# Performance work log

Hardware: AMD Instinct MI355X
Metric: run time of the kernel (lower is better)

## Reference

```python
import jax, jax.numpy as jnp
import numpy as np

DEPTH, DIM, HEADS, DHEAD, MLP, CTX_DIM = 4, 1024, 16, 64, 4096, 1024
INNER = HEADS * DHEAD
SCALE = DHEAD ** -0.5
B, N, M = 4, 1024, 2048


def setup_inputs() -> dict:
    key = jax.random.key(0)
    ks = jax.random.split(key, 16)
    w = lambda k, shape: jax.random.normal(k, shape, dtype=jnp.float32) * 0.02
    return {
        "x": jax.random.normal(ks[0], (B, N, DIM), dtype=jnp.float32),
        "context": jax.random.normal(ks[1], (B, M, CTX_DIM), dtype=jnp.float32),
        "mask": jnp.ones((B, N), dtype=jnp.int32),
        # LayerNorm params: index 0 = pre-self-attn, 1 = pre-cross-attn, 2 = pre-FFN
        "ln_g": jnp.ones((DEPTH, 3, DIM), dtype=jnp.float32),
        "ln_b": jnp.zeros((DEPTH, 3, DIM), dtype=jnp.float32),
        "Wqkv": w(ks[2], (DEPTH, DIM, 3 * INNER)),
        "Wo_sa": w(ks[3], (DEPTH, INNER, DIM)),
        "bo_sa": jnp.zeros((DEPTH, DIM), dtype=jnp.float32),
        "Wkv": w(ks[4], (DEPTH, CTX_DIM, 2 * INNER)),
        "Wq": w(ks[5], (DEPTH, DIM, INNER)),
        "Wo_ca": w(ks[6], (DEPTH, INNER, DIM)),
        "bo_ca": jnp.zeros((DEPTH, DIM), dtype=jnp.float32),
        "W1": w(ks[7], (DEPTH, DIM, MLP)),
        "b1": jnp.zeros((DEPTH, MLP), dtype=jnp.float32),
        "W2": w(ks[8], (DEPTH, MLP, DIM)),
        "b2": jnp.zeros((DEPTH, DIM), dtype=jnp.float32),
    }


def _ln(x, g, b, eps=1e-5):
    mu = jnp.mean(x, axis=-1, keepdims=True)
    var = jnp.var(x, axis=-1, keepdims=True)
    return (x - mu) * jax.lax.rsqrt(var + eps) * g + b


def _split_heads(t):  # [b, n, h*d] -> [b, h, n, d]
    b, n, _ = t.shape
    return t.reshape(b, n, HEADS, DHEAD).transpose(0, 2, 1, 3)


def _merge_heads(t):  # [b, h, n, d] -> [b, n, h*d]
    b, h, n, d = t.shape
    return t.transpose(0, 2, 1, 3).reshape(b, n, h * d)


def _forward(x, context, mask, ln_g, ln_b, Wqkv, Wo_sa, bo_sa, Wkv, Wq, Wo_ca, bo_ca, W1, b1, W2, b2):
    neg_mask = (1 - mask).astype(x.dtype)  # [b, n]
    for i in range(DEPTH):
        # ---- self-attention (PreNorm) ----
        h = _ln(x, ln_g[i, 0], ln_b[i, 0])
        qkv = h @ Wqkv[i]
        q, k, v = jnp.split(qkv, 3, axis=-1)
        q, k, v = _split_heads(q), _split_heads(k), _split_heads(v)
        dots = jnp.einsum('bhnd,bhmd->bhnm', q, k) * SCALE
        dots = dots - neg_mask[:, None, None, :] * 1e11  # mask over keys
        attn = jax.nn.softmax(dots, axis=-1)
        out = _merge_heads(jnp.einsum('bhnm,bhmd->bhnd', attn, v))
        x = x + out @ Wo_sa[i] + bo_sa[i]
        # ---- cross-attention (PreNorm) ----
        h = _ln(x, ln_g[i, 1], ln_b[i, 1])
        kv = context @ Wkv[i]
        k, v = jnp.split(kv, 2, axis=-1)
        q = _split_heads(h @ Wq[i])
        k, v = _split_heads(k), _split_heads(v)
        dots = jnp.einsum('bhnd,bhmd->bhnm', q, k) * SCALE  # [b, h, n, m]
        dots = dots - neg_mask[:, None, :, None] * 1e6  # mask over queries
        attn = jax.nn.softmax(dots, axis=-1)
        out = _merge_heads(jnp.einsum('bhnm,bhmd->bhnd', attn, v))
        x = x + out @ Wo_ca[i] + bo_ca[i]
        # ---- feed-forward (PreNorm) ----
        h = _ln(x, ln_g[i, 2], ln_b[i, 2])
        h = jax.nn.gelu(h @ W1[i] + b1[i], approximate=False)
        x = x + h @ W2[i] + b2[i]
    return x


def reference(x, context, mask, ln_g, ln_b, Wqkv, Wo_sa, bo_sa, Wkv, Wq, Wo_ca, bo_ca, W1, b1, W2, b2):
    return _forward(x, context, mask, ln_g, ln_b, Wqkv, Wo_sa, bo_sa, Wkv, Wq, Wo_ca, bo_ca, W1, b1, W2, b2)
```

## Files before the change

### kernel.cpp

```cpp
#include <hip/hip_runtime.h>
#include <math.h>

#define DEPTH_ 4
#define DIM_ 1024
#define HEADS_ 16
#define DHEAD_ 64
#define MLP_ 4096
#define CTX_ 1024
#define INNER_ 1024
#define B_ 4
#define N_ 1024
#define M_ 2048

typedef unsigned short u16;
typedef __attribute__((ext_vector_type(4))) unsigned short u16x4;
typedef __attribute__((ext_vector_type(8))) short bf16x8;
typedef __attribute__((ext_vector_type(4))) float f32x4;
typedef __attribute__((ext_vector_type(4))) int i32x4;

#define SCQ 0.18033688011112042f

__device__ __forceinline__ u16 f2bf(float f) {
    unsigned u = __float_as_uint(f);
    return (u16)((u + 0x7fffu + ((u >> 16) & 1u)) >> 16);
}

__device__ __forceinline__ float bf2f(u16 v) {
    return __uint_as_float(((unsigned)v) << 16);
}

__device__ __forceinline__ float exp2_fast(float x) {
    float r;
    asm("v_exp_f32 %0, %1" : "=v"(r) : "v"(x));
    return r;
}

__device__ __forceinline__ float rcp_fast(float x) {
    float r;
    asm("v_rcp_f32 %0, %1" : "=v"(r) : "v"(x));
    return r;
}

__device__ __forceinline__ float max3f(float a, float b, float c) {
    float r;
    asm("v_max3_f32 %0, %1, %2, %3" : "=v"(r) : "v"(a), "v"(b), "v"(c));
    return r;
}

__device__ __forceinline__ unsigned cvt_pk_bf16(float lo, float hi) {
    unsigned r;
    asm("v_cvt_pk_bf16_f32 %0, %1, %2" : "=v"(r) : "v"(lo), "v"(hi));
    return r;
}

__device__ __forceinline__ float gelu_fast(float v) {
    float t = v + 0.044715f * v * v * v;
    float e = exp2_fast(-2.302221673f * t);
    return v * rcp_fast(1.0f + e);
}

__device__ __forceinline__ int kv_sigma(int kv) {
    return (kv & ~31) | (((kv >> 2) & 3) << 3) | (((kv >> 4) & 1) << 2) |
           (kv & 3);
}

#define GLOAD16(gp, sp)                                                        \
    __builtin_amdgcn_global_load_lds(                                          \
        (const __attribute__((address_space(1))) void*)(gp),                   \
        (__attribute__((address_space(3))) void*)(sp), 16, 0, 0)

template <int MODE>
__global__ __launch_bounds__(256) void ln_res(
    u16* __restrict__ xb, const u16* __restrict__ d0,
    const u16* __restrict__ d1, const float* __restrict__ dbias,
    const float* __restrict__ g, const float* __restrict__ b,
    u16* __restrict__ y) {
    int row = blockIdx.x;
    u16x4 xv = ((const u16x4*)(xb + (size_t)row * DIM_))[threadIdx.x];
    float4 v = {bf2f(xv[0]), bf2f(xv[1]), bf2f(xv[2]), bf2f(xv[3])};
    if constexpr (MODE == 1) {
        u16x4 a0 = ((const u16x4*)(d0 + (size_t)row * DIM_))[threadIdx.x];
        u16x4 a1 = ((const u16x4*)(d1 + (size_t)row * DIM_))[threadIdx.x];
        float4 bb4 = ((const float4*)dbias)[threadIdx.x];
        v.x += bf2f(a0[0]) + bf2f(a1[0]) + bb4.x;
        v.y += bf2f(a0[1]) + bf2f(a1[1]) + bb4.y;
        v.z += bf2f(a0[2]) + bf2f(a1[2]) + bb4.z;
        v.w += bf2f(a0[3]) + bf2f(a1[3]) + bb4.w;
        u16x4 xo = {f2bf(v.x), f2bf(v.y), f2bf(v.z), f2bf(v.w)};
        ((u16x4*)(xb + (size_t)row * DIM_))[threadIdx.x] = xo;
    }
    float s  = v.x + v.y + v.z + v.w;
    float ss = v.x * v.x + v.y * v.y + v.z * v.z + v.w * v.w;
    #pragma unroll
    for (int off = 32; off; off >>= 1) {
        s  += __shfl_down(s, off);
        ss += __shfl_down(ss, off);
    }
    __shared__ float red[10];
    int wid = threadIdx.x >> 6, lane = threadIdx.x & 63;
    if (lane == 0) { red[wid] = s; red[4 + wid] = ss; }
    __syncthreads();
    if (threadIdx.x == 0) {
        float ts  = red[0] + red[1] + red[2] + red[3];
        float tss = red[4] + red[5] + red[6] + red[7];
        float mu  = ts * (1.0f / DIM_);
        float var = tss * (1.0f / DIM_) - mu * mu;
        red[8] = mu;
        red[9] = rsqrtf(var + 1e-5f);
    }
    __syncthreads();
    float mu = red[8], rs = red[9];
    float4 gg = ((const float4*)g)[threadIdx.x];
    float4 bb = ((const float4*)b)[threadIdx.x];
    u16x4 o;
    o[0] = f2bf((v.x - mu) * rs * gg.x + bb.x);
    o[1] = f2bf((v.y - mu) * rs * gg.y + bb.y);
    o[2] = f2bf((v.z - mu) * rs * gg.z + bb.z);
    o[3] = f2bf((v.w - mu) * rs * gg.w + bb.w);
    ((u16x4*)(y + (size_t)row * DIM_))[threadIdx.x] = o;
}

__global__ __launch_bounds__(256) void res_add(
    float* __restrict__ xout, const u16* __restrict__ xb,
    const u16* __restrict__ d0, const u16* __restrict__ d1,
    const float* __restrict__ dbias) {
    int row = blockIdx.x;
    u16x4 xv = ((const u16x4*)(xb + (size_t)row * DIM_))[threadIdx.x];
    u16x4 a0 = ((const u16x4*)(d0 + (size_t)row * DIM_))[threadIdx.x];
    u16x4 a1 = ((const u16x4*)(d1 + (size_t)row * DIM_))[threadIdx.x];
    float4 bb4 = ((const float4*)dbias)[threadIdx.x];
    float4 v;
    v.x = bf2f(xv[0]) + bf2f(a0[0]) + bf2f(a1[0]) + bb4.x;
    v.y = bf2f(xv[1]) + bf2f(a0[1]) + bf2f(a1[1]) + bb4.y;
    v.z = bf2f(xv[2]) + bf2f(a0[2]) + bf2f(a1[2]) + bb4.z;
    v.w = bf2f(xv[3]) + bf2f(a0[3]) + bf2f(a1[3]) + bb4.w;
    ((float4*)(xout + (size_t)row * DIM_))[threadIdx.x] = v;
}

__global__ __launch_bounds__(256) void cast_kernel(const float* __restrict__ in,
                                                   u16* __restrict__ out) {
    int i = blockIdx.x * 256 + threadIdx.x;
    float4 v = ((const float4*)in)[i];
    u16x4 o = {f2bf(v.x), f2bf(v.y), f2bf(v.z), f2bf(v.w)};
    ((u16x4*)out)[i] = o;
}

struct PrepArgs {
    const float* src[7];
    int K[7];
    int N[7];
    int dstOff[7];
    int tileCum[7];
};

__global__ __launch_bounds__(256) void prep_weights(PrepArgs a,
                                                    u16* __restrict__ wt) {
    __shared__ float tile[32][33];
    int bid = blockIdx.x;
    int wi = 0;
    while (bid >= a.tileCum[wi]) ++wi;
    int tbase = wi ? a.tileCum[wi - 1] : 0;
    int tid = bid - tbase;
    int Kd = a.K[wi], Nd = a.N[wi];
    int ntx = Nd >> 5;
    int bx = (tid % ntx) * 32;
    int by = (tid / ntx) * 32;
    const float* W = a.src[wi];
    u16* Wt = wt + a.dstOff[wi];

    int t = threadIdx.x;
    int kl = t >> 3, n4 = (t & 7) * 4;
    float4 v = *(const float4*)(W + (size_t)(by + kl) * Nd + bx + n4);
    tile[kl][n4 + 0] = v.x; tile[kl][n4 + 1] = v.y;
    tile[kl][n4 + 2] = v.z; tile[kl][n4 + 3] = v.w;
    __syncthreads();
    int nl = t >> 3, k4 = (t & 7) * 4;
    u16x4 o;
    #pragma unroll
    for (int j = 0; j < 4; ++j) o[j] = f2bf(tile[k4 + j][nl]);
    *(u16x4*)(Wt + (size_t)(bx + nl) * Kd + by + k4) = o;
}

template <int EPI, int SPLITK>
__global__ __launch_bounds__(256, 3) void gemm_mfma3(
    const u16* __restrict__ A, const u16* __restrict__ Bt,
    const float* __restrict__ bias, void* __restrict__ Cout,
    u16* __restrict__ vt, int Mdim, int Ndim, int Kdim, int nx, int ny) {
    __shared__ __align__(16) u16 As[3][128 * 32];
    __shared__ __align__(16) u16 Bs[3][128 * 32];
    const int t = threadIdx.x;
    const int lane = t & 63, w = t >> 6;
    const int c = lane & 15, g = lane >> 4;
    const int wy = w >> 1, wx = w & 1;

    const int nwg = gridDim.x;
    const int wid = (blockIdx.x & 7) * (nwg >> 3) + (blockIdx.x >> 3);
    const int bx = wid % nx;
    const int by = (wid / nx) % ny;
    const int bz = wid / (nx * ny);
    const int m0 = by * 128, n0 = bx * 128;

    f32x4 acc[4][4] = {};

    const int srow = w * 32 + (lane >> 2);
    const int scb  = (((lane & 3) ^ ((srow >> 1) & 3)) * 8);
    const u16* Ag = A + (size_t)(m0 + srow) * Kdim + scb;
    const u16* Bg = Bt + (size_t)(n0 + srow) * Kdim + scb;

    auto stage = [&](int buf, int k0) {
        GLOAD16(Ag + k0, &As[buf][w * 1024]);
        GLOAD16(Ag + k0 + (size_t)16 * Kdim, &As[buf][w * 1024 + 512]);
        GLOAD16(Bg + k0, &Bs[buf][w * 1024]);
        GLOAD16(Bg + k0 + (size_t)16 * Kdim, &Bs[buf][w * 1024 + 512]);
    };
    const int rsw = (c >> 1) & 3;
    auto compute = [&](int buf) {
        bf16x8 a[4], b[4];
        #pragma unroll
        for (int i = 0; i < 4; ++i)
            a[i] = *(const bf16x8*)&As[buf][(wy * 64 + i * 16 + c) * 32 +
                                            ((g ^ rsw) * 8)];
        #pragma unroll
        for (int j = 0; j < 4; ++j)
            b[j] = *(const bf16x8*)&Bs[buf][(wx * 64 + j * 16 + c) * 32 +
                                            ((g ^ rsw) * 8)];
        __builtin_amdgcn_s_setprio(1);
        #pragma unroll
        for (int i = 0; i < 4; ++i)
            #pragma unroll
            for (int j = 0; j < 4; ++j)
                acc[i][j] = __builtin_amdgcn_mfma_f32_16x16x32_bf16(
                    a[i], b[j], acc[i][j], 0, 0, 0);
        __builtin_amdgcn_s_setprio(0);
    };

    const int kchunk = Kdim / SPLITK;
    const int kbeg = bz * kchunk;
    const int nsteps = kchunk / 32;

    stage(0, kbeg);
    stage(1, kbeg + 32);
    int cb = 0, sb = 2;
    for (int s = 0; s < nsteps; ++s) {
        if (s + 1 < nsteps)
            asm volatile("s_waitcnt vmcnt(4)" ::: "memory");
        else
            asm volatile("s_waitcnt vmcnt(0)" ::: "memory");
        __builtin_amdgcn_s_barrier();
        if (s + 2 < nsteps) {
            stage(sb, kbeg + (s + 2) * 32);
            sb = (sb == 2) ? 0 : sb + 1;
        }
        compute(cb);
        cb = (cb == 2) ? 0 : cb + 1;
    }

    const size_t outOff = (SPLITK > 1) ? (size_t)bz * Mdim * Ndim : 0;

    #pragma unroll
    for (int i = 0; i < 4; ++i) {
        int row0 = m0 + wy * 64 + i * 16 + g * 4;
        #pragma unroll
        for (int j = 0; j < 4; ++j) {
            int col = n0 + wx * 64 + j * 16 + c;
            u16x4 o4;
            #pragma unroll
            for (int r = 0; r < 4; ++r) {
                float v = acc[i][j][r];
                size_t idx = (size_t)(row0 + r) * Ndim + col;
                if constexpr (EPI == 0) {
                    ((u16*)Cout)[outOff + idx] = f2bf(v);
                } else if constexpr (EPI == 4) {
                    if (col < 1024) v *= SCQ;
                    u16 bv = f2bf(v);
                    ((u16*)Cout)[idx] = bv;
                    o4[r] = bv;
                } else if constexpr (EPI == 1) {
                    v += bias[col];
                    ((u16*)Cout)[idx] = f2bf(gelu_fast(v));
                }
            }
            if constexpr (EPI == 4) {
                if (n0 + wx * 64 + j * 16 >= 2048) {
                    int hh = (col - 2048) >> 6;
                    int dd = col & 63;
                    int bi = row0 / 1024;
                    int kv = row0 % 1024;
                    int kvs = kv_sigma(kv);
                    *(u16x4*)&vt[(((size_t)bi * HEADS_ + hh) * 64 + dd) * 1024 +
                                 kvs] = o4;
                }
            }
        }
    }
}

__global__ __launch_bounds__(256, 3) void gemm_dual(
    const u16* __restrict__ Akv, const u16* __restrict__ Btkv,
    u16* __restrict__ Ckv, u16* __restrict__ vt,
    const u16* __restrict__ Aq, const u16* __restrict__ Btq,
    u16* __restrict__ Cq) {
    __shared__ __align__(16) u16 As[3][128 * 32];
    __shared__ __align__(16) u16 Bs[3][128 * 32];
    const int t = threadIdx.x;
    const int lane = t & 63, w = t >> 6;
    const int c = lane & 15, g = lane >> 4;
    const int wy = w >> 1, wx = w & 1;
    const int Kdim = 1024;

    const int nwg = gridDim.x;
    const int wid = (blockIdx.x & 7) * (nwg >> 3) + (blockIdx.x >> 3);
    const bool pkv = wid < 1024;
    const u16* A;
    const u16* Bt;
    u16* Cc;
    int Ndim, bx, by;
    if (pkv) {
        A = Akv; Bt = Btkv; Cc = Ckv; Ndim = 2048;
        bx = wid & 15; by = wid >> 4;
    } else {
        int w2 = wid - 1024;
        A = Aq; Bt = Btq; Cc = Cq; Ndim = 1024;
        bx = w2 & 7; by = w2 >> 3;
    }
    const int m0 = by * 128, n0 = bx * 128;

    f32x4 acc[4][4] = {};

    const int srow = w * 32 + (lane >> 2);
    const int scb  = (((lane & 3) ^ ((srow >> 1) & 3)) * 8);
    const u16* Ag = A + (size_t)(m0 + srow) * Kdim + scb;
    const u16* Bg = Bt + (size_t)(n0 + srow) * Kdim + scb;

    auto stage = [&](int buf, int k0) {
        GLOAD16(Ag + k0, &As[buf][w * 1024]);
        GLOAD16(Ag + k0 + (size_t)16 * Kdim, &As[buf][w * 1024 + 512]);
        GLOAD16(Bg + k0, &Bs[buf][w * 1024]);
        GLOAD16(Bg + k0 + (size_t)16 * Kdim, &Bs[buf][w * 1024 + 512]);
    };
    const int rsw = (c >> 1) & 3;
    auto compute = [&](int buf) {
        bf16x8 a[4], b[4];
        #pragma unroll
        for (int i = 0; i < 4; ++i)
            a[i] = *(const bf16x8*)&As[buf][(wy * 64 + i * 16 + c) * 32 +
                                            ((g ^ rsw) * 8)];
        #pragma unroll
        for (int j = 0; j < 4; ++j)
            b[j] = *(const bf16x8*)&Bs[buf][(wx * 64 + j * 16 + c) * 32 +
                                            ((g ^ rsw) * 8)];
        __builtin_amdgcn_s_setprio(1);
        #pragma unroll
        for (int i = 0; i < 4; ++i)
            #pragma unroll
            for (int j = 0; j < 4; ++j)
                acc[i][j] = __builtin_amdgcn_mfma_f32_16x16x32_bf16(
                    a[i], b[j], acc[i][j], 0, 0, 0);
        __builtin_amdgcn_s_setprio(0);
    };

    stage(0, 0);
    stage(1, 32);
    int cb = 0, sb = 2;
    const int nsteps = 32;
    for (int s = 0; s < nsteps; ++s) {
        if (s + 1 < nsteps)
            asm volatile("s_waitcnt vmcnt(4)" ::: "memory");
        else
            asm volatile("s_waitcnt vmcnt(0)" ::: "memory");
        __builtin_amdgcn_s_barrier();
        if (s + 2 < nsteps) {
            stage(sb, (s + 2) * 32);
            sb = (sb == 2) ? 0 : sb + 1;
        }
        compute(cb);
        cb = (cb == 2) ? 0 : cb + 1;
    }

    #pragma unroll
    for (int i = 0; i < 4; ++i) {
        int row0 = m0 + wy * 64 + i * 16 + g * 4;
        #pragma unroll
        for (int j = 0; j < 4; ++j) {
            int col = n0 + wx * 64 + j * 16 + c;
            u16x4 o4;
            #pragma unroll
            for (int r = 0; r < 4; ++r) {
                float v = acc[i][j][r];
                size_t idx = (size_t)(row0 + r) * Ndim + col;
                if (pkv) {
                    u16 bv = f2bf(v);
                    Cc[idx] = bv;
                    o4[r] = bv;
                } else {
                    Cc[idx] = f2bf(v * SCQ);
                }
            }
            if (pkv && (n0 + wx * 64 + j * 16 >= 1024)) {
                int hh = (col - 1024) >> 6;
                int dd = col & 63;
                int bi = row0 / 2048;
                int kv = row0 % 2048;
                int kvs = kv_sigma(kv);
                *(u16x4*)&vt[(((size_t)bi * HEADS_ + hh) * 64 + dd) * 2048 +
                             kvs] = o4;
            }
        }
    }
}

template <int KLEN, int IS_SA>
__global__ __launch_bounds__(256) void attn_mfma2(
    const u16* __restrict__ Qsrc, const u16* __restrict__ Ksrc,
    const u16* __restrict__ Vtg, const int* __restrict__ mask,
    u16* __restrict__ O) {
    constexpr int QSTR = IS_SA ? 3 * INNER_ : INNER_;
    constexpr int KSTR = IS_SA ? 3 * INNER_ : 2 * INNER_;
    constexpr int KOFF = IS_SA ? INNER_ : 0;

    __shared__ __align__(16) u16 Ks[2][64 * 64];
    __shared__ __align__(16) u16 Vs[2][64 * 64];

    const int t = threadIdx.x;
    const int lane = t & 63, w = t >> 6;
    const int c = lane & 15, g = lane >> 4;

    const int nwg = gridDim.x;
    const int wid = (blockIdx.x & 7) * (nwg >> 3) + (blockIdx.x >> 3);
    const int qb = wid & 15;
    const int h  = (wid >> 4) & 15;
    const int bb = wid >> 8;
    const int q0 = qb * 64;
    const int kvbase = bb * KLEN;

    const u16* qp =
        Qsrc + (size_t)(bb * N_ + q0 + w * 16 + c) * QSTR + h * 64 + g * 8;
    bf16x8 qf[2];
    qf[0] = *(const bf16x8*)qp;
    qf[1] = *(const bf16x8*)(qp + 32);

    const int sl_r = lane >> 3;
    const int scol = ((lane & 7) ^ sl_r) * 8;
    const int r0 = w * 16, r1 = w * 16 + 8;
    const u16* kp0 = Ksrc + (size_t)(kvbase + r0 + sl_r) * KSTR + KOFF +
                     h * 64 + scol;
    const u16* kp1 = Ksrc + (size_t)(kvbase + r1 + sl_r) * KSTR + KOFF +
                     h * 64 + scol;
    const u16* vp0 =
        Vtg + ((size_t)(bb * HEADS_ + h) * 64 + r0 + sl_r) * KLEN + scol;
    const u16* vp1 =
        Vtg + ((size_t)(bb * HEADS_ + h) * 64 + r1 + sl_r) * KLEN + scol;
    const int* mp = mask + bb * N_ + lane;

    auto stageKV = [&](int buf) {
        GLOAD16(kp0, &Ks[buf][r0 * 64]);
        GLOAD16(kp1, &Ks[buf][r1 * 64]);
        GLOAD16(vp0, &Vs[buf][r0 * 64]);
        GLOAD16(vp1, &Vs[buf][r1 * 64]);
        kp0 += (size_t)64 * KSTR;
        kp1 += (size_t)64 * KSTR;
        vp0 += 64;
        vp1 += 64;
    };

    f32x4 o[4] = {};
    f32x4 oL = {};
    float mr = -1e30f;
    const i32x4 onesI = {0x3F803F80, 0x3F803F80, 0x3F803F80, 0x3F803F80};
    const bf16x8 ones = *(const bf16x8*)&onesI;
    constexpr int NT = KLEN / 64;

    stageKV(0);
    __syncthreads();
    int cur = 0;

    for (int kt = 0; kt < NT; ++kt) {
        if (kt + 1 < NT) stageKV(cur ^ 1);

        f32x4 sv[4] = {};
        #pragma unroll
        for (int kvb = 0; kvb < 4; ++kvb) {
            #pragma unroll
            for (int f = 0; f < 2; ++f) {
                bf16x8 kf = *(const bf16x8*)&Ks[cur][(kvb * 16 + c) * 64 +
                                                     (((g + 4 * f) ^ (c & 7)) * 8)];
                sv[kvb] = __builtin_amdgcn_mfma_f32_16x16x32_bf16(
                    kf, qf[f], sv[kvb], 0, 0, 0);
            }
        }

        if constexpr (IS_SA) {
            int mbit = *mp;
            mp += 64;
            unsigned long long ball = __ballot(mbit != 0);
            if (ball != ~0ull) {
                float negm_reg = mbit ? 0.f : 2.0e10f;
                #pragma unroll
                for (int kvb = 0; kvb < 4; ++kvb)
                    #pragma unroll
                    for (int r = 0; r < 4; ++r)
                        sv[kvb][r] -= __shfl(negm_reg, kvb * 16 + g * 4 + r);
            }
        }

        float x0 = max3f(sv[0][0], sv[0][1], sv[0][2]);
        float x1 = max3f(sv[0][3], sv[1][0], sv[1][1]);
        float x2 = max3f(sv[1][2], sv[1][3], sv[2][0]);
        float x3 = max3f(sv[2][1], sv[2][2], sv[2][3]);
        float x4 = max3f(sv[3][0], sv[3][1], sv[3][2]);
        float tm = fmaxf(max3f(x0, x1, x2), max3f(x3, x4, sv[3][3]));

        if (!__all(tm - mr <= 8.0f)) {
            float tmc = fmaxf(tm, __shfl_xor(tm, 16));
            tmc = fmaxf(tmc, __shfl_xor(tmc, 32));
            float mn = fmaxf(mr, tmc);
            float corr = exp2_fast(mr - mn);
            mr = mn;
            float corrO[4];
            #pragma unroll
            for (int r = 0; r < 4; ++r) corrO[r] = __shfl(corr, g * 4 + r);
            #pragma unroll
            for (int db = 0; db < 4; ++db)
                #pragma unroll
                for (int r = 0; r < 4; ++r) o[db][r] *= corrO[r];
            #pragma unroll
            for (int r = 0; r < 4; ++r) oL[r] *= corrO[r];
        }

        #pragma unroll
        for (int kvb = 0; kvb < 4; ++kvb)
            #pragma unroll
            for (int r = 0; r < 4; ++r)
                sv[kvb][r] = exp2_fast(sv[kvb][r] - mr);

        unsigned pk[4][2];
        #pragma unroll
        for (int kvb = 0; kvb < 4; ++kvb)
            #pragma unroll
            for (int j = 0; j < 2; ++j)
                pk[kvb][j] = cvt_pk_bf16(sv[kvb][2 * j], sv[kvb][2 * j + 1]);

        #pragma unroll
        for (int pv = 0; pv < 2; ++pv) {
            i32x4 tw = {(int)pk[2 * pv][0], (int)pk[2 * pv][1],
                        (int)pk[2 * pv + 1][0], (int)pk[2 * pv + 1][1]};
            bf16x8 pa = *(bf16x8*)&tw;
            oL = __builtin_amdgcn_mfma_f32_16x16x32_bf16(pa, ones, oL, 0, 0, 0);
            #pragma unroll
            for (int db = 0; db < 4; ++db) {
                bf16x8 vf = *(const bf16x8*)&Vs[cur][(db * 16 + c) * 64 +
                                                     (((g + 4 * pv) ^ (c & 7)) * 8)];
                o[db] = __builtin_amdgcn_mfma_f32_16x16x32_bf16(pa, vf, o[db],
                                                                0, 0, 0);
            }
        }
        __syncthreads();
        cur ^= 1;
    }

    float invO[4];
    #pragma unroll
    for (int r = 0; r < 4; ++r) invO[r] = rcp_fast(oL[r]);
    #pragma unroll
    for (int db = 0; db < 4; ++db)
        #pragma unroll
        for (int r = 0; r < 4; ++r) {
            size_t idx =
                (size_t)(bb * N_ + q0 + w * 16 + g * 4 + r) * INNER_ +
                h * 64 + db * 16 + c;
            O[idx] = f2bf(o[db][r] * invO[r]);
        }
}

extern "C" void kernel_launch(void* const* d_in, const int* in_sizes, int n_in,
                              void* d_out, int out_size, void* d_ws,
                              size_t ws_size, hipStream_t stream) {
    const float* x     = (const float*)d_in[0];
    const float* ctx   = (const float*)d_in[1];
    const int*   mask  = (const int*)d_in[2];
    const float* ln_g  = (const float*)d_in[3];
    const float* ln_b  = (const float*)d_in[4];
    const float* Wqkv  = (const float*)d_in[5];
    const float* Wo_sa = (const float*)d_in[6];
    const float* bo_sa = (const float*)d_in[7];
    const float* Wkv   = (const float*)d_in[8];
    const float* Wq    = (const float*)d_in[9];
    const float* Wo_ca = (const float*)d_in[10];
    const float* bo_ca = (const float*)d_in[11];
    const float* W1    = (const float*)d_in[12];
    const float* b1    = (const float*)d_in[13];
    const float* W2    = (const float*)d_in[14];
    const float* b2    = (const float*)d_in[15];
    float* xout = (float*)d_out;

    char* ws = (char*)d_ws;
    u16* lnout = (u16*)ws;
    u16* big   = (u16*)(ws + (8ull << 20));
    u16* qca   = (u16*)(ws + (40ull << 20));
    u16* ctxb  = (u16*)(ws + (48ull << 20));
    u16* wt    = (u16*)(ws + (64ull << 20));
    u16* xb    = (u16*)(ws + (96ull << 20));
    u16* R1    = (u16*)(ws + (104ull << 20));
    u16* aout  = lnout;

    const int O_QKV = 0;
    const int O_WOSA = 3145728;
    const int O_WQ   = 4194304;
    const int O_WKV  = 5242880;
    const int O_WOCA = 7340032;
    const int O_W1   = 8388608;
    const int O_W2   = 12582912;

    cast_kernel<<<B_ * M_ * CTX_ / 1024, 256, 0, stream>>>(ctx, ctxb);
    cast_kernel<<<B_ * N_ * DIM_ / 1024, 256, 0, stream>>>(x, xb);

    const int ROWS = B_ * N_;
    const int HALF = ROWS * DIM_;
    dim3 blk(256);

    for (int i = 0; i < DEPTH_; ++i) {
        const float* g  = ln_g + (size_t)(i * 3) * DIM_;
        const float* bb = ln_b + (size_t)(i * 3) * DIM_;

        PrepArgs pa;
        pa.src[0] = Wqkv  + (size_t)i * DIM_ * 3 * INNER_;
        pa.src[1] = Wo_sa + (size_t)i * INNER_ * DIM_;
        pa.src[2] = Wq    + (size_t)i * DIM_ * INNER_;
        pa.src[3] = Wkv   + (size_t)i * CTX_ * 2 * INNER_;
        pa.src[4] = Wo_ca + (size_t)i * INNER_ * DIM_;
        pa.src[5] = W1    + (size_t)i * DIM_ * MLP_;
        pa.src[6] = W2    + (size_t)i * MLP_ * DIM_;
        int Ks_[7] = {1024, 1024, 1024, 1024, 1024, 1024, 4096};
        int Ns_[7] = {3072, 1024, 1024, 2048, 1024, 4096, 1024};
        int Of_[7] = {O_QKV, O_WOSA, O_WQ, O_WKV, O_WOCA, O_W1, O_W2};
        int cum = 0;
        for (int k = 0; k < 7; ++k) {
            pa.K[k] = Ks_[k]; pa.N[k] = Ns_[k]; pa.dstOff[k] = Of_[k];
            cum += (Ks_[k] / 32) * (Ns_[k] / 32);
            pa.tileCum[k] = cum;
        }
        prep_weights<<<cum, blk, 0, stream>>>(pa, wt);

        if (i == 0)
            ln_res<0><<<ROWS, blk, 0, stream>>>(xb, nullptr, nullptr,
                                                nullptr, g, bb, lnout);
        else
            ln_res<1><<<ROWS, blk, 0, stream>>>(xb, R1, R1 + HALF,
                                                b2 + (size_t)(i - 1) * DIM_,
                                                g, bb, lnout);
        gemm_mfma3<4, 1><<<24 * 32, blk, 0, stream>>>(
            lnout, wt + O_QKV, nullptr, big, R1, ROWS, 3 * INNER_, DIM_,
            24, 32);
        attn_mfma2<N_, 1><<<1024, blk, 0, stream>>>(big, big, R1, mask,
                                                    aout);
        gemm_mfma3<0, 2><<<8 * 32 * 2, blk, 0, stream>>>(
            aout, wt + O_WOSA, nullptr, R1, nullptr, ROWS, DIM_, INNER_,
            8, 32);

        ln_res<1><<<ROWS, blk, 0, stream>>>(xb, R1, R1 + HALF,
                                            bo_sa + (size_t)i * DIM_,
                                            g + DIM_, bb + DIM_, lnout);
        gemm_dual<<<1280, blk, 0, stream>>>(ctxb, wt + O_WKV, big, R1,
                                            lnout, wt + O_WQ, qca);
        attn_mfma2<M_, 0><<<1024, blk, 0, stream>>>(qca, big, R1, mask,
                                                    aout);
        gemm_mfma3<0, 2><<<8 * 32 * 2, blk, 0, stream>>>(
            aout, wt + O_WOCA, nullptr, R1, nullptr, ROWS, DIM_, INNER_,
            8, 32);

        ln_res<1><<<ROWS, blk, 0, stream>>>(xb, R1, R1 + HALF,
                                            bo_ca + (size_t)i * DIM_,
                                            g + 2 * DIM_, bb + 2 * DIM_,
                                            lnout);
        gemm_mfma3<1, 1><<<32 * 32, blk, 0, stream>>>(
            lnout, wt + O_W1, b1 + (size_t)i * MLP_, big, nullptr, ROWS, MLP_,
            DIM_, 32, 32);
        gemm_mfma3<0, 2><<<8 * 32 * 2, blk, 0, stream>>>(
            big, wt + O_W2, nullptr, R1, nullptr, ROWS, DIM_, MLP_, 8, 32);
    }
    res_add<<<ROWS, blk, 0, stream>>>(xout, xb, R1, R1 + HALF,
                                      b2 + (size_t)(DEPTH_ - 1) * DIM_);
}
```

Before: 1.514 ms.

## Triple-buffer attention K/V staging and skip writing unused V rows

The attention kernel moves from double to triple buffered LDS staging of K/V tiles. It keeps two tiles in flight, waits with vmcnt counters and uses one barrier per iteration instead of two __syncthreads. The QKV and KV projection epilogues stop writing the row-major V columns, which are only read through the transposed vt buffer, cutting global store traffic. The cost is more LDS per block, which may lower occupancy, and a hand-tuned vmcnt count that must match the number of loads stageKV issues.

```diff
diff --git a/kernel.cpp b/kernel.cpp
--- a/kernel.cpp
+++ b/kernel.cpp
@@ -271,10 +271,13 @@
                 if constexpr (EPI == 0) {
                     ((u16*)Cout)[outOff + idx] = f2bf(v);
                 } else if constexpr (EPI == 4) {
-                    if (col < 1024) v *= SCQ;
-                    u16 bv = f2bf(v);
-                    ((u16*)Cout)[idx] = bv;
-                    o4[r] = bv;
+                    if (col < 1024) {
+                        ((u16*)Cout)[idx] = f2bf(v * SCQ);
+                    } else if (col < 2048) {
+                        ((u16*)Cout)[idx] = f2bf(v);
+                    } else {
+                        o4[r] = f2bf(v);
+                    }
                 } else if constexpr (EPI == 1) {
                     v += bias[col];
                     ((u16*)Cout)[idx] = f2bf(gelu_fast(v));
@@ -390,7 +393,7 @@
                 size_t idx = (size_t)(row0 + r) * Ndim + col;
                 if (pkv) {
                     u16 bv = f2bf(v);
-                    Cc[idx] = bv;
+                    if (col < 1024) Cc[idx] = bv;
                     o4[r] = bv;
                 } else {
                     Cc[idx] = f2bf(v * SCQ);
@@ -418,8 +421,8 @@
     constexpr int KSTR = IS_SA ? 3 * INNER_ : 2 * INNER_;
     constexpr int KOFF = IS_SA ? INNER_ : 0;
 
-    __shared__ __align__(16) u16 Ks[2][64 * 64];
-    __shared__ __align__(16) u16 Vs[2][64 * 64];
+    __shared__ __align__(16) u16 Ks[3][64 * 64];
+    __shared__ __align__(16) u16 Vs[3][64 * 64];
 
     const int t = threadIdx.x;
     const int lane = t & 63, w = t >> 6;
@@ -471,19 +474,27 @@
     constexpr int NT = KLEN / 64;
 
     stageKV(0);
-    __syncthreads();
-    int cur = 0;
+    stageKV(1);
+    int cb = 0, sb = 2;
 
     for (int kt = 0; kt < NT; ++kt) {
-        if (kt + 1 < NT) stageKV(cur ^ 1);
+        if (kt + 1 < NT)
+            asm volatile("s_waitcnt vmcnt(4)" ::: "memory");
+        else
+            asm volatile("s_waitcnt vmcnt(0)" ::: "memory");
+        __builtin_amdgcn_s_barrier();
+        if (kt + 2 < NT) {
+            stageKV(sb);
+            sb = (sb == 2) ? 0 : sb + 1;
+        }
 
         f32x4 sv[4] = {};
         #pragma unroll
         for (int kvb = 0; kvb < 4; ++kvb) {
             #pragma unroll
             for (int f = 0; f < 2; ++f) {
-                bf16x8 kf = *(const bf16x8*)&Ks[cur][(kvb * 16 + c) * 64 +
-                                                     (((g + 4 * f) ^ (c & 7)) * 8)];
+                bf16x8 kf = *(const bf16x8*)&Ks[cb][(kvb * 16 + c) * 64 +
+                                                    (((g + 4 * f) ^ (c & 7)) * 8)];
                 sv[kvb] = __builtin_amdgcn_mfma_f32_16x16x32_bf16(
                     kf, qf[f], sv[kvb], 0, 0, 0);
             }
@@ -548,14 +559,13 @@
             oL = __builtin_amdgcn_mfma_f32_16x16x32_bf16(pa, ones, oL, 0, 0, 0);
             #pragma unroll
             for (int db = 0; db < 4; ++db) {
-                bf16x8 vf = *(const bf16x8*)&Vs[cur][(db * 16 + c) * 64 +
-                                                     (((g + 4 * pv) ^ (c & 7)) * 8)];
+                bf16x8 vf = *(const bf16x8*)&Vs[cb][(db * 16 + c) * 64 +
+                                                    (((g + 4 * pv) ^ (c & 7)) * 8)];
                 o[db] = __builtin_amdgcn_mfma_f32_16x16x32_bf16(pa, vf, o[db],
                                                                 0, 0, 0);
             }
         }
-        __syncthreads();
-        cur ^= 1;
+        cb = (cb == 2) ? 0 : cb + 1;
     }
 
     float invO[4];
```

Result: slower. 1.546 ms (+2.1%).
